# Optimization experiments

Measured on AMD Instinct MI355X. Metric: run time of the kernel, lower is better.

## Reference

```python
import jax, jax.numpy as jnp
import numpy as np

N, T, U = 8, 200, 50
ENC_DIM = DEC_DIM = JOIN_DIM = 512
VOCAB = 500


def setup_inputs() -> dict:
    key = jax.random.key(0)
    ks = jax.random.split(key, 8)
    s_enc = 1.0 / np.sqrt(ENC_DIM)
    s_dec = 1.0 / np.sqrt(DEC_DIM)
    s_out = 1.0 / np.sqrt(JOIN_DIM)
    return {
        "encoder_out": jax.random.normal(ks[0], (N, T, ENC_DIM), jnp.float32),
        "decoder_out": jax.random.normal(ks[1], (N, U, DEC_DIM), jnp.float32),
        "W_enc": jax.random.normal(ks[2], (JOIN_DIM, ENC_DIM), jnp.float32) * s_enc,
        "b_enc": jax.random.normal(ks[3], (JOIN_DIM,), jnp.float32) * 0.01,
        "W_dec": jax.random.normal(ks[4], (JOIN_DIM, DEC_DIM), jnp.float32) * s_dec,
        "b_dec": jax.random.normal(ks[5], (JOIN_DIM,), jnp.float32) * 0.01,
        "W_out": jax.random.normal(ks[6], (VOCAB, JOIN_DIM), jnp.float32) * s_out,
        "b_out": jax.random.normal(ks[7], (VOCAB,), jnp.float32) * 0.01,
    }


def reference(encoder_out, decoder_out, W_enc, b_enc, W_dec, b_dec, W_out, b_out):
    # Input projections (ScaledLinear == Linear at execution time)
    enc = jnp.einsum("ntc,jc->ntj", encoder_out, W_enc) + b_enc  # (N,T,J)
    dec = jnp.einsum("nuc,jc->nuj", decoder_out, W_dec) + b_dec  # (N,U,J)
    # Broadcast add over (T,U), tanh, then output linear -> (N,T,U,V)
    x = jnp.tanh(enc[:, :, None, :] + dec[:, None, :, :])
    logits = jnp.einsum("ntuj,vj->ntuv", x, W_out) + b_out
    return logits
```

## Files before the change

kernel.cpp:

```cpp
#include <hip/hip_runtime.h>
#include <hip/hip_bf16.h>

typedef __bf16 bf16x8 __attribute__((ext_vector_type(8)));
typedef unsigned short ushort8 __attribute__((ext_vector_type(8)));
typedef unsigned short ushort4v __attribute__((ext_vector_type(4)));
typedef float f32x4 __attribute__((ext_vector_type(4)));

__device__ __forceinline__ unsigned short f2bf(float f) {
    union { float f; unsigned int i; } v;
    v.f = f;
    unsigned int i = v.i;
    i += 0x7fffu + ((i >> 16) & 1u);
    return (unsigned short)(i >> 16);
}

union bfcast { ushort8 u; bf16x8 b; };

__device__ __forceinline__ bf16x8 load_w8_f32(const float* p) {
    const float4 f0 = *(const float4*)p;
    const float4 f1 = *(const float4*)(p + 4);
    bfcast c;
    c.u[0] = f2bf(f0.x); c.u[1] = f2bf(f0.y); c.u[2] = f2bf(f0.z); c.u[3] = f2bf(f0.w);
    c.u[4] = f2bf(f1.x); c.u[5] = f2bf(f1.y); c.u[6] = f2bf(f1.z); c.u[7] = f2bf(f1.w);
    return c.b;
}

__device__ __forceinline__ float fast_tanh(float x) {
    float e = __expf(2.0f * x);
    return 1.0f - 2.0f * __builtin_amdgcn_rcpf(e + 1.0f);
}

__global__ __launch_bounds__(256, 2) void prep_kernel(
    const float* __restrict__ enc_in, const float* __restrict__ dec_in,
    const float* __restrict__ W_enc,  const float* __restrict__ b_enc,
    const float* __restrict__ W_dec,  const float* __restrict__ b_dec,
    const float* __restrict__ W_out,
    float* __restrict__ enc_proj, float* __restrict__ dec_proj,
    unsigned short* __restrict__ wout_bf)
{
    const int blk = blockIdx.x;
    const int tid = threadIdx.x;

    if (blk >= 252) {
        const int e = (blk - 252) * 1024 + tid * 4;
        ushort4v p;
        if (e < 256000) {
            const float4 v = *(const float4*)(W_out + e);
            p.x = f2bf(v.x); p.y = f2bf(v.y); p.z = f2bf(v.z); p.w = f2bf(v.w);
        } else {
            p.x = 0; p.y = 0; p.z = 0; p.w = 0;
        }
        *(ushort4v*)(wout_bf + e) = p;
        return;
    }

    const float *A, *W, *bias; float* outp; int Ma, t, jq;
    if (blk < 200) { A = enc_in; W = W_enc; bias = b_enc; outp = enc_proj;
                     Ma = 1600; t = blk >> 2; jq = blk & 3; }
    else           { const int b2 = blk - 200;
                     A = dec_in; W = W_dec; bias = b_dec; outp = dec_proj;
                     Ma = 400;  t = b2 >> 2;  jq = b2 & 3; }
    const int r0 = t * 32;

    __shared__ unsigned short tile[32 * 520];
    {
        const int row = tid >> 3, q = tid & 7;
        int gr = r0 + row;
        if (gr >= Ma) gr = Ma - 1;
        const float* src = A + (size_t)gr * 512;
        ushort8* dst = (ushort8*)(tile + row * 520);
        #pragma unroll
        for (int i = 0; i < 8; ++i) {
            const int c = q + i * 8;
            const int k = c * 8;
            const float4 a0 = *(const float4*)(src + k);
            const float4 a1 = *(const float4*)(src + k + 4);
            bfcast pk;
            pk.u[0] = f2bf(a0.x); pk.u[1] = f2bf(a0.y); pk.u[2] = f2bf(a0.z); pk.u[3] = f2bf(a0.w);
            pk.u[4] = f2bf(a1.x); pk.u[5] = f2bf(a1.y); pk.u[6] = f2bf(a1.z); pk.u[7] = f2bf(a1.w);
            dst[c] = pk.u;
        }
    }
    __syncthreads();

    const int wave = tid >> 6, lane = tid & 63;
    const int lrow = lane & 15;
    const int lk8  = (lane >> 4) * 8;
    const int j0   = jq * 128 + wave * 32;

    f32x4 acc[2][2];
    #pragma unroll
    for (int mi = 0; mi < 2; ++mi)
        #pragma unroll
        for (int ji = 0; ji < 2; ++ji)
            acc[mi][ji] = (f32x4){0.f, 0.f, 0.f, 0.f};

    const unsigned short* abase = tile + lrow * 520 + lk8;
    const float* wb0 = W + (size_t)(j0 + lrow) * 512 + lk8;
    const float* wb1 = wb0 + 16 * 512;

    #pragma unroll
    for (int kk = 0; kk < 512; kk += 32) {
        const bf16x8 a0 = *(const bf16x8*)(abase + kk);
        const bf16x8 a1 = *(const bf16x8*)(abase + 16 * 520 + kk);
        const bf16x8 b0 = load_w8_f32(wb0 + kk);
        const bf16x8 b1 = load_w8_f32(wb1 + kk);
        acc[0][0] = __builtin_amdgcn_mfma_f32_16x16x32_bf16(a0, b0, acc[0][0], 0, 0, 0);
        acc[0][1] = __builtin_amdgcn_mfma_f32_16x16x32_bf16(a0, b1, acc[0][1], 0, 0, 0);
        acc[1][0] = __builtin_amdgcn_mfma_f32_16x16x32_bf16(a1, b0, acc[1][0], 0, 0, 0);
        acc[1][1] = __builtin_amdgcn_mfma_f32_16x16x32_bf16(a1, b1, acc[1][1], 0, 0, 0);
    }

    const int crow = (lane >> 4) * 4;
    const int ccol = lane & 15;
    #pragma unroll
    for (int ji = 0; ji < 2; ++ji) {
        const int col = j0 + ji * 16 + ccol;
        const float bv = bias[col];
        #pragma unroll
        for (int mi = 0; mi < 2; ++mi)
            #pragma unroll
            for (int rg = 0; rg < 4; ++rg) {
                const int gr = r0 + mi * 16 + crow + rg;
                if (gr < Ma) outp[(size_t)gr * 512 + col] = acc[mi][ji][rg] + bv;
            }
    }
}

__global__ __launch_bounds__(512, 4) void joiner_kernel(
    const float* __restrict__ encp,
    const float* __restrict__ decp,
    const unsigned short* __restrict__ Wout,
    const float* __restrict__ bout,
    float* __restrict__ out)
{
    __shared__ float4 smem[4160];
    unsigned short* tile = (unsigned short*)smem;
    const int tid = threadIdx.x;
    const int r0 = blockIdx.x * 64;

    {
        const int row = tid >> 3, q = tid & 7;
        const int r = r0 + row;
        const int n = r / 10000;
        const int rem = r % 10000;
        const int t = rem / 50;
        const int u = rem - t * 50;
        const float* erow = encp + (size_t)(n * 200 + t) * 512;
        const float* drow = decp + (size_t)(n * 50 + u) * 512;
        ushort8* dst = (ushort8*)(tile + row * 520);
        #pragma unroll
        for (int i = 0; i < 8; ++i) {
            const int c = q + i * 8;
            const int k = c * 8;
            const float4 ev0 = *(const float4*)(erow + k);
            const float4 ev1 = *(const float4*)(erow + k + 4);
            const float4 dv0 = *(const float4*)(drow + k);
            const float4 dv1 = *(const float4*)(drow + k + 4);
            float xs[8] = {ev0.x + dv0.x, ev0.y + dv0.y, ev0.z + dv0.z, ev0.w + dv0.w,
                           ev1.x + dv1.x, ev1.y + dv1.y, ev1.z + dv1.z, ev1.w + dv1.w};
            bfcast pk;
            #pragma unroll
            for (int j = 0; j < 8; ++j) pk.u[j] = f2bf(fast_tanh(xs[j]));
            dst[c] = pk.u;
        }
    }
    __syncthreads();

    const int wave = tid >> 6, lane = tid & 63;
    const int lrow = lane & 15;
    const int lk8  = (lane >> 4) * 8;
    const int v0   = wave * 64;

    f32x4 acc[4][4];
    #pragma unroll
    for (int mi = 0; mi < 4; ++mi)
        #pragma unroll
        for (int ji = 0; ji < 4; ++ji)
            acc[mi][ji] = (f32x4){0.f, 0.f, 0.f, 0.f};

    const unsigned short* wrow[4];
    #pragma unroll
    for (int ji = 0; ji < 4; ++ji)
        wrow[ji] = Wout + (size_t)(v0 + ji * 16 + lrow) * 512 + lk8;
    const unsigned short* abase = tile + lrow * 520 + lk8;

    bf16x8 breg[2][4];
    #pragma unroll
    for (int ji = 0; ji < 4; ++ji) breg[0][ji] = *(const bf16x8*)(wrow[ji]);
    #pragma unroll
    for (int ji = 0; ji < 4; ++ji) breg[1][ji] = *(const bf16x8*)(wrow[ji] + 32);

    #pragma unroll
    for (int kk = 0; kk < 16; ++kk) {
        bf16x8 a[4];
        #pragma unroll
        for (int mi = 0; mi < 4; ++mi)
            a[mi] = *(const bf16x8*)(abase + mi * 16 * 520 + kk * 32);
        bf16x8 bn[4];
        if (kk < 14) {
            #pragma unroll
            for (int ji = 0; ji < 4; ++ji)
                bn[ji] = *(const bf16x8*)(wrow[ji] + (kk + 2) * 32);
        }
        #pragma unroll
        for (int mi = 0; mi < 4; ++mi)
            #pragma unroll
            for (int ji = 0; ji < 4; ++ji)
                acc[mi][ji] = __builtin_amdgcn_mfma_f32_16x16x32_bf16(
                    a[mi], breg[kk & 1][ji], acc[mi][ji], 0, 0, 0);
        if (kk < 14) {
            #pragma unroll
            for (int ji = 0; ji < 4; ++ji) breg[kk & 1][ji] = bn[ji];
        }
    }

    float* ob = (float*)smem;
    const int crow = (lane >> 4) * 4;
    const int ccol = lane & 15;
    const int srow = tid >> 4, sslot = tid & 15;
    #pragma unroll
    for (int h = 0; h < 2; ++h) {
        __syncthreads();
        #pragma unroll
        for (int mi2 = 0; mi2 < 2; ++mi2) {
            const int mi = h * 2 + mi2;
            #pragma unroll
            for (int ji = 0; ji < 4; ++ji) {
                const int v = v0 + ji * 16 + ccol;
                const float bv = (v < 500) ? bout[v] : 0.f;
                #pragma unroll
                for (int rg = 0; rg < 4; ++rg)
                    ob[(mi2 * 16 + crow + rg) * 516 + v] = acc[mi][ji][rg] + bv;
            }
        }
        __syncthreads();
        const size_t gr = (size_t)(r0 + h * 32 + srow);
        const float* src = ob + srow * 516;
        float* drow = out + gr * 500;
        #pragma unroll
        for (int i = 0; i < 8; ++i) {
            const int c = sslot + 16 * i;
            if (c < 125)
                *(float4*)(drow + c * 4) = *(const float4*)(src + c * 4);
        }
    }
}

extern "C" void kernel_launch(void* const* d_in, const int* in_sizes, int n_in,
                              void* d_out, int out_size, void* d_ws, size_t ws_size,
                              hipStream_t stream) {
    (void)in_sizes; (void)n_in; (void)out_size; (void)ws_size;
    const float* enc_in = (const float*)d_in[0];
    const float* dec_in = (const float*)d_in[1];
    const float* W_enc  = (const float*)d_in[2];
    const float* b_enc  = (const float*)d_in[3];
    const float* W_dec  = (const float*)d_in[4];
    const float* b_dec  = (const float*)d_in[5];
    const float* W_out  = (const float*)d_in[6];
    const float* b_out  = (const float*)d_in[7];
    float* out = (float*)d_out;

    float* ws = (float*)d_ws;
    float* enc_proj = ws;
    float* dec_proj = ws + 819200;
    unsigned short* wout_bf = (unsigned short*)(ws + 1024000);

    hipLaunchKernelGGL(prep_kernel, dim3(508), dim3(256), 0, stream,
                       enc_in, dec_in, W_enc, b_enc, W_dec, b_dec, W_out,
                       enc_proj, dec_proj, wout_bf);
    hipLaunchKernelGGL(joiner_kernel, dim3(1250), dim3(512), 0, stream,
                       enc_proj, dec_proj, wout_bf, b_out, out);
}
```

Measured before the change: 260.8 us.

## Halve joiner row tile, raise occupancy, and remap blocks per XCD

The joiner kernel now handles 32 rows per block instead of 64. This halves shared memory and accumulator registers, doubles the grid, and raises the launch-bounds occupancy hint from 4 to 6. Block indices are remapped so each XCD processes a contiguous range of rows, which is meant to improve L2 locality for the encoder and decoder projection rows. The cost is that W_out is re-read twice as often per output row, and the weight prefetch depth drops from two k-steps to one, which may expose more load latency.

```diff
diff --git a/kernel.cpp b/kernel.cpp
--- a/kernel.cpp
+++ b/kernel.cpp
@@ -127,20 +127,25 @@
     }
 }
 
-__global__ __launch_bounds__(512, 4) void joiner_kernel(
+__global__ __launch_bounds__(512, 6) void joiner_kernel(
     const float* __restrict__ encp,
     const float* __restrict__ decp,
     const unsigned short* __restrict__ Wout,
     const float* __restrict__ bout,
     float* __restrict__ out)
 {
-    __shared__ float4 smem[4160];
+    __shared__ float4 smem[2080];
     unsigned short* tile = (unsigned short*)smem;
     const int tid = threadIdx.x;
-    const int r0 = blockIdx.x * 64;
+
+    const int orig = blockIdx.x;
+    const int xcd  = orig & 7;
+    const int i8   = orig >> 3;
+    const int blk  = (xcd < 4 ? xcd * 313 : 1252 + (xcd - 4) * 312) + i8;
+    const int r0 = blk * 32;
 
     {
-        const int row = tid >> 3, q = tid & 7;
+        const int row = tid >> 4, q = tid & 15;
         const int r = r0 + row;
         const int n = r / 10000;
         const int rem = r % 10000;
@@ -150,8 +155,8 @@
         const float* drow = decp + (size_t)(n * 50 + u) * 512;
         ushort8* dst = (ushort8*)(tile + row * 520);
         #pragma unroll
-        for (int i = 0; i < 8; ++i) {
-            const int c = q + i * 8;
+        for (int i = 0; i < 4; ++i) {
+            const int c = q + i * 16;
             const int k = c * 8;
             const float4 ev0 = *(const float4*)(erow + k);
             const float4 ev1 = *(const float4*)(erow + k + 4);
@@ -172,75 +177,64 @@
     const int lk8  = (lane >> 4) * 8;
     const int v0   = wave * 64;
 
-    f32x4 acc[4][4];
-    #pragma unroll
-    for (int mi = 0; mi < 4; ++mi)
+    f32x4 acc[2][4];
+    #pragma unroll
+    for (int mi = 0; mi < 2; ++mi)
         #pragma unroll
         for (int ji = 0; ji < 4; ++ji)
             acc[mi][ji] = (f32x4){0.f, 0.f, 0.f, 0.f};
 
-    const unsigned short* wrow[4];
+    const unsigned short* abase = tile + lrow * 520 + lk8;
+    const unsigned short* wbase = Wout + (size_t)(v0 + lrow) * 512 + lk8;
+
+    bf16x8 breg[4];
     #pragma unroll
     for (int ji = 0; ji < 4; ++ji)
-        wrow[ji] = Wout + (size_t)(v0 + ji * 16 + lrow) * 512 + lk8;
-    const unsigned short* abase = tile + lrow * 520 + lk8;
-
-    bf16x8 breg[2][4];
-    #pragma unroll
-    for (int ji = 0; ji < 4; ++ji) breg[0][ji] = *(const bf16x8*)(wrow[ji]);
-    #pragma unroll
-    for (int ji = 0; ji < 4; ++ji) breg[1][ji] = *(const bf16x8*)(wrow[ji] + 32);
+        breg[ji] = *(const bf16x8*)(wbase + ji * 8192);
 
     #pragma unroll
     for (int kk = 0; kk < 16; ++kk) {
-        bf16x8 a[4];
-        #pragma unroll
-        for (int mi = 0; mi < 4; ++mi)
-            a[mi] = *(const bf16x8*)(abase + mi * 16 * 520 + kk * 32);
+        const bf16x8 a0 = *(const bf16x8*)(abase + kk * 32);
+        const bf16x8 a1 = *(const bf16x8*)(abase + 16 * 520 + kk * 32);
         bf16x8 bn[4];
-        if (kk < 14) {
+        if (kk < 15) {
             #pragma unroll
             for (int ji = 0; ji < 4; ++ji)
-                bn[ji] = *(const bf16x8*)(wrow[ji] + (kk + 2) * 32);
-        }
-        #pragma unroll
-        for (int mi = 0; mi < 4; ++mi)
-            #pragma unroll
-            for (int ji = 0; ji < 4; ++ji)
-                acc[mi][ji] = __builtin_amdgcn_mfma_f32_16x16x32_bf16(
-                    a[mi], breg[kk & 1][ji], acc[mi][ji], 0, 0, 0);
-        if (kk < 14) {
-            #pragma unroll
-            for (int ji = 0; ji < 4; ++ji) breg[kk & 1][ji] = bn[ji];
+                bn[ji] = *(const bf16x8*)(wbase + ji * 8192 + (kk + 1) * 32);
+        }
+        #pragma unroll
+        for (int ji = 0; ji < 4; ++ji) {
+            acc[0][ji] = __builtin_amdgcn_mfma_f32_16x16x32_bf16(a0, breg[ji], acc[0][ji], 0, 0, 0);
+            acc[1][ji] = __builtin_amdgcn_mfma_f32_16x16x32_bf16(a1, breg[ji], acc[1][ji], 0, 0, 0);
+        }
+        if (kk < 15) {
+            #pragma unroll
+            for (int ji = 0; ji < 4; ++ji) breg[ji] = bn[ji];
         }
     }
 
     float* ob = (float*)smem;
     const int crow = (lane >> 4) * 4;
     const int ccol = lane & 15;
-    const int srow = tid >> 4, sslot = tid & 15;
+    const int srow = tid >> 5, sslot = tid & 31;
     #pragma unroll
     for (int h = 0; h < 2; ++h) {
         __syncthreads();
         #pragma unroll
-        for (int mi2 = 0; mi2 < 2; ++mi2) {
-            const int mi = h * 2 + mi2;
-            #pragma unroll
-            for (int ji = 0; ji < 4; ++ji) {
-                const int v = v0 + ji * 16 + ccol;
-                const float bv = (v < 500) ? bout[v] : 0.f;
-                #pragma unroll
-                for (int rg = 0; rg < 4; ++rg)
-                    ob[(mi2 * 16 + crow + rg) * 516 + v] = acc[mi][ji][rg] + bv;
-            }
+        for (int ji = 0; ji < 4; ++ji) {
+            const int v = v0 + ji * 16 + ccol;
+            const float bv = (v < 500) ? bout[v] : 0.f;
+            #pragma unroll
+            for (int rg = 0; rg < 4; ++rg)
+                ob[(crow + rg) * 516 + v] = acc[h][ji][rg] + bv;
         }
         __syncthreads();
-        const size_t gr = (size_t)(r0 + h * 32 + srow);
+        const size_t gr = (size_t)(r0 + h * 16 + srow);
         const float* src = ob + srow * 516;
         float* drow = out + gr * 500;
         #pragma unroll
-        for (int i = 0; i < 8; ++i) {
-            const int c = sslot + 16 * i;
+        for (int i = 0; i < 4; ++i) {
+            const int c = sslot + 32 * i;
             if (c < 125)
                 *(float4*)(drow + c * 4) = *(const float4*)(src + c * 4);
         }
@@ -269,6 +263,6 @@
     hipLaunchKernelGGL(prep_kernel, dim3(508), dim3(256), 0, stream,
                        enc_in, dec_in, W_enc, b_enc, W_dec, b_dec, W_out,
                        enc_proj, dec_proj, wout_bf);
-    hipLaunchKernelGGL(joiner_kernel, dim3(1250), dim3(512), 0, stream,
+    hipLaunchKernelGGL(joiner_kernel, dim3(2500), dim3(512), 0, stream,
                        enc_proj, dec_proj, wout_bf, b_out, out);
 }
```

Result: slower. 333.7 us (+27.9%).

## Double-buffer tanh A-tile in K chunks to overlap with MFMA and shrink LDS

Applied to the files above, without the earlier changes.

Splits the K=512 activation tile into four 128-wide chunks held in a two-slot LDS buffer, so the tanh/bf16 conversion of the next chunk runs alongside the MFMAs on the current chunk. LDS per block drops from about 66KB to about 35KB, which should let more blocks share a CU. The W_out register double-buffer prefetch is removed, the output staging is redone in four 16-row passes, and an extra barrier per chunk is added.

```diff
diff --git a/kernel.cpp b/kernel.cpp
--- a/kernel.cpp
+++ b/kernel.cpp
@@ -134,35 +134,31 @@
     const float* __restrict__ bout,
     float* __restrict__ out)
 {
-    __shared__ float4 smem[4160];
-    unsigned short* tile = (unsigned short*)smem;
+    __shared__ unsigned short buf[2][64 * 136];
     const int tid = threadIdx.x;
     const int r0 = blockIdx.x * 64;
 
+    const int trow = tid >> 3, tq = tid & 7;
+    const int r_ = r0 + trow;
+    const int n_ = r_ / 10000;
+    const int rem_ = r_ % 10000;
+    const int t_ = rem_ / 50;
+    const int u_ = rem_ - t_ * 50;
+    const float* erow = encp + (size_t)(n_ * 200 + t_) * 512 + tq * 16;
+    const float* drow = decp + (size_t)(n_ * 50 + u_) * 512 + tq * 16;
+
     {
-        const int row = tid >> 3, q = tid & 7;
-        const int r = r0 + row;
-        const int n = r / 10000;
-        const int rem = r % 10000;
-        const int t = rem / 50;
-        const int u = rem - t * 50;
-        const float* erow = encp + (size_t)(n * 200 + t) * 512;
-        const float* drow = decp + (size_t)(n * 50 + u) * 512;
-        ushort8* dst = (ushort8*)(tile + row * 520);
-        #pragma unroll
-        for (int i = 0; i < 8; ++i) {
-            const int c = q + i * 8;
-            const int k = c * 8;
-            const float4 ev0 = *(const float4*)(erow + k);
-            const float4 ev1 = *(const float4*)(erow + k + 4);
-            const float4 dv0 = *(const float4*)(drow + k);
-            const float4 dv1 = *(const float4*)(drow + k + 4);
-            float xs[8] = {ev0.x + dv0.x, ev0.y + dv0.y, ev0.z + dv0.z, ev0.w + dv0.w,
-                           ev1.x + dv1.x, ev1.y + dv1.y, ev1.z + dv1.z, ev1.w + dv1.w};
-            bfcast pk;
-            #pragma unroll
-            for (int j = 0; j < 8; ++j) pk.u[j] = f2bf(fast_tanh(xs[j]));
-            dst[c] = pk.u;
+        unsigned short* nb = &buf[0][0] + trow * 136 + tq * 16;
+        #pragma unroll
+        for (int p = 0; p < 4; ++p) {
+            const float4 ev = *(const float4*)(erow + p * 4);
+            const float4 dv = *(const float4*)(drow + p * 4);
+            ushort4v pk;
+            pk.x = f2bf(fast_tanh(ev.x + dv.x));
+            pk.y = f2bf(fast_tanh(ev.y + dv.y));
+            pk.z = f2bf(fast_tanh(ev.z + dv.z));
+            pk.w = f2bf(fast_tanh(ev.w + dv.w));
+            *(ushort4v*)(nb + p * 4) = pk;
         }
     }
     __syncthreads();
@@ -183,66 +179,67 @@
     #pragma unroll
     for (int ji = 0; ji < 4; ++ji)
         wrow[ji] = Wout + (size_t)(v0 + ji * 16 + lrow) * 512 + lk8;
-    const unsigned short* abase = tile + lrow * 520 + lk8;
-
-    bf16x8 breg[2][4];
-    #pragma unroll
-    for (int ji = 0; ji < 4; ++ji) breg[0][ji] = *(const bf16x8*)(wrow[ji]);
-    #pragma unroll
-    for (int ji = 0; ji < 4; ++ji) breg[1][ji] = *(const bf16x8*)(wrow[ji] + 32);
-
-    #pragma unroll
-    for (int kk = 0; kk < 16; ++kk) {
-        bf16x8 a[4];
-        #pragma unroll
-        for (int mi = 0; mi < 4; ++mi)
-            a[mi] = *(const bf16x8*)(abase + mi * 16 * 520 + kk * 32);
-        bf16x8 bn[4];
-        if (kk < 14) {
+
+    #pragma unroll
+    for (int c = 0; c < 4; ++c) {
+        const unsigned short* cb = &buf[c & 1][0] + lrow * 136 + lk8;
+        unsigned short* nb = &buf[(c + 1) & 1][0] + trow * 136 + tq * 16;
+        const int co = c * 128;
+        const int go = (c + 1) * 128;
+        #pragma unroll
+        for (int kk = 0; kk < 4; ++kk) {
+            if (c < 3) {
+                const float4 ev = *(const float4*)(erow + go + kk * 4);
+                const float4 dv = *(const float4*)(drow + go + kk * 4);
+                ushort4v pk;
+                pk.x = f2bf(fast_tanh(ev.x + dv.x));
+                pk.y = f2bf(fast_tanh(ev.y + dv.y));
+                pk.z = f2bf(fast_tanh(ev.z + dv.z));
+                pk.w = f2bf(fast_tanh(ev.w + dv.w));
+                *(ushort4v*)(nb + kk * 4) = pk;
+            }
+            bf16x8 b[4];
             #pragma unroll
             for (int ji = 0; ji < 4; ++ji)
-                bn[ji] = *(const bf16x8*)(wrow[ji] + (kk + 2) * 32);
-        }
-        #pragma unroll
-        for (int mi = 0; mi < 4; ++mi)
-            #pragma unroll
-            for (int ji = 0; ji < 4; ++ji)
-                acc[mi][ji] = __builtin_amdgcn_mfma_f32_16x16x32_bf16(
-                    a[mi], breg[kk & 1][ji], acc[mi][ji], 0, 0, 0);
-        if (kk < 14) {
-            #pragma unroll
-            for (int ji = 0; ji < 4; ++ji) breg[kk & 1][ji] = bn[ji];
-        }
-    }
-
-    float* ob = (float*)smem;
+                b[ji] = *(const bf16x8*)(wrow[ji] + co + kk * 32);
+            bf16x8 a[4];
+            #pragma unroll
+            for (int mi = 0; mi < 4; ++mi)
+                a[mi] = *(const bf16x8*)(cb + mi * 16 * 136 + kk * 32);
+            #pragma unroll
+            for (int mi = 0; mi < 4; ++mi)
+                #pragma unroll
+                for (int ji = 0; ji < 4; ++ji)
+                    acc[mi][ji] = __builtin_amdgcn_mfma_f32_16x16x32_bf16(
+                        a[mi], b[ji], acc[mi][ji], 0, 0, 0);
+        }
+        __syncthreads();
+    }
+
+    float* ob = (float*)&buf[0][0];
     const int crow = (lane >> 4) * 4;
     const int ccol = lane & 15;
-    const int srow = tid >> 4, sslot = tid & 15;
-    #pragma unroll
-    for (int h = 0; h < 2; ++h) {
+    const int srow = tid >> 5, sslot = tid & 31;
+    #pragma unroll
+    for (int h = 0; h < 4; ++h) {
+        if (h) __syncthreads();
+        #pragma unroll
+        for (int ji = 0; ji < 4; ++ji) {
+            const int v = v0 + ji * 16 + ccol;
+            const float bv = (v < 500) ? bout[v] : 0.f;
+            #pragma unroll
+            for (int rg = 0; rg < 4; ++rg)
+                ob[(crow + rg) * 516 + v] = acc[h][ji][rg] + bv;
+        }
         __syncthreads();
-        #pragma unroll
-        for (int mi2 = 0; mi2 < 2; ++mi2) {
-            const int mi = h * 2 + mi2;
-            #pragma unroll
-            for (int ji = 0; ji < 4; ++ji) {
-                const int v = v0 + ji * 16 + ccol;
-                const float bv = (v < 500) ? bout[v] : 0.f;
-                #pragma unroll
-                for (int rg = 0; rg < 4; ++rg)
-                    ob[(mi2 * 16 + crow + rg) * 516 + v] = acc[mi][ji][rg] + bv;
-            }
-        }
-        __syncthreads();
-        const size_t gr = (size_t)(r0 + h * 32 + srow);
+        const size_t gr = (size_t)(r0 + h * 16 + srow);
         const float* src = ob + srow * 516;
-        float* drow = out + gr * 500;
-        #pragma unroll
-        for (int i = 0; i < 8; ++i) {
-            const int c = sslot + 16 * i;
-            if (c < 125)
-                *(float4*)(drow + c * 4) = *(const float4*)(src + c * 4);
+        float* drw = out + gr * 500;
+        #pragma unroll
+        for (int i = 0; i < 4; ++i) {
+            const int c2 = sslot + 32 * i;
+            if (c2 < 125)
+                *(float4*)(drw + c2 * 4) = *(const float4*)(src + c2 * 4);
         }
     }
 }
```

Measured after the change: 274.7 us. 5.3% more time.
